# Performance work log

Measured on AMD Instinct MI355X. Metric: run time of the kernel, lower is better.

## Reference

```python
import jax, jax.numpy as jnp
import numpy as np

HEAD_NUM = 16
D_MODEL = 1024
D_K = D_MODEL // HEAD_NUM


def setup_inputs() -> dict:
    key = jax.random.key(0)
    ks = jax.random.split(key, 11)
    B, S = 4, 2048
    def xavier(k, shape):
        fan_in, fan_out = shape[1], shape[0]
        lim = np.sqrt(6.0 / (fan_in + fan_out))
        return jax.random.uniform(k, shape, jnp.float32, -lim, lim)
    return {
        "query": jax.random.normal(ks[0], (B, S, D_MODEL), jnp.float32),
        "key": jax.random.normal(ks[1], (B, S, D_MODEL), jnp.float32),
        "value": jax.random.normal(ks[2], (B, S, D_MODEL), jnp.float32),
        "w_q": xavier(ks[3], (D_MODEL, D_MODEL)),
        "b_q": jnp.zeros((D_MODEL,), jnp.float32),
        "w_k": xavier(ks[4], (D_MODEL, D_MODEL)),
        "b_k": jnp.zeros((D_MODEL,), jnp.float32),
        "w_v": xavier(ks[5], (D_MODEL, D_MODEL)),
        "b_v": jnp.zeros((D_MODEL,), jnp.float32),
        "w_o": xavier(ks[6], (D_MODEL, D_MODEL)),
        "b_o": jnp.zeros((D_MODEL,), jnp.float32),
    }


def reference(query, key, value, w_q, b_q, w_k, b_k, w_v, b_v, w_o, b_o):
    B = query.shape[0]
    # Linear projections (torch Linear: x @ W^T + b), split into heads: [B,H,S,Dk]
    def proj(x, w, b):
        y = x @ w.T + b
        return y.reshape(B, -1, HEAD_NUM, D_K).transpose(0, 2, 1, 3)
    q = proj(query, w_q, b_q)
    k = proj(key, w_k, b_k)
    v = proj(value, w_v, b_v)
    # scaled dot-product attention with full score matrix [B,H,Sq,Sk]
    scores = jnp.einsum('bhqd,bhkd->bhqk', q, k) / jnp.sqrt(jnp.float32(D_K))
    attn = jax.nn.softmax(scores, axis=-1)
    out = jnp.einsum('bhqk,bhkd->bhqd', attn, v)
    out = out.transpose(0, 2, 1, 3).reshape(B, -1, HEAD_NUM * D_K)
    return out @ w_o.T + b_o
```

## Files before the change

kernel.cpp:

```cpp
#include <hip/hip_runtime.h>
#include <hip/hip_bf16.h>
#include <stdint.h>

#define HN 16
#define DMODEL 1024
#define DKH 64
#define SEQ 2048

typedef __attribute__((ext_vector_type(8))) short short8v;
typedef __attribute__((ext_vector_type(4))) short short4v;
typedef __attribute__((ext_vector_type(4))) float f32x4;

__device__ __forceinline__ short bfc(float x) {
    __hip_bfloat16 h = __float2bfloat16(x);
    return *reinterpret_cast<short*>(&h);
}

__device__ __forceinline__ void gll16(const void* g, void* l) {
    __builtin_amdgcn_global_load_lds(
        (const __attribute__((address_space(1))) unsigned int*)g,
        (__attribute__((address_space(3))) unsigned int*)l, 16, 0, 0);
}

__global__ void cvtw_kernel(const float* __restrict__ w0, const float* __restrict__ w1,
                            const float* __restrict__ w2, const float* __restrict__ w3,
                            short* __restrict__ dst, float scale0) {
    const int z = blockIdx.z;
    const float* src = z == 0 ? w0 : z == 1 ? w1 : z == 2 ? w2 : w3;
    short* d = dst + ((size_t)z << 20);
    const float scale = (z == 0) ? scale0 : 1.f;
    const int i = blockIdx.x * blockDim.x + threadIdx.x;
    const float4 v0 = ((const float4*)src)[i * 2];
    const float4 v1 = ((const float4*)src)[i * 2 + 1];
    short8v o;
    o[0] = bfc(v0.x * scale); o[1] = bfc(v0.y * scale);
    o[2] = bfc(v0.z * scale); o[3] = bfc(v0.w * scale);
    o[4] = bfc(v1.x * scale); o[5] = bfc(v1.y * scale);
    o[6] = bfc(v1.z * scale); o[7] = bfc(v1.w * scale);
    ((short8v*)d)[i] = o;
}

__global__ __launch_bounds__(256) void gemm_proj(
    const float* __restrict__ xq, const float* __restrict__ xk, const float* __restrict__ xv,
    const short* __restrict__ wb,
    const float* __restrict__ bq, const float* __restrict__ bk, const float* __restrict__ bv,
    short* __restrict__ qb, short* __restrict__ kb, short* __restrict__ vtb, float c1)
{
    constexpr int K = DMODEL;
    const int z = blockIdx.z;
    const float* A    = z == 0 ? xq : z == 1 ? xk : xv;
    const short* W    = wb + ((size_t)z << 20);
    const float* bias = z == 0 ? bq : z == 1 ? bk : bv;
    const float bscale = (z == 0) ? c1 : 1.f;

    __shared__ __align__(16) short As[128][72];
    __shared__ __align__(16) short Bs[128][64];
    const int t = threadIdx.x, lane = t & 63;
    const int w = t >> 6, wr = w >> 1, wc = w & 1;
    const int m0 = blockIdx.y * 128, n0 = blockIdx.x * 128;
    const int r16 = lane & 15, g = lane >> 4;

    f32x4 acc[4][4];
    #pragma unroll
    for (int i = 0; i < 4; ++i)
        #pragma unroll
        for (int j = 0; j < 4; ++j) { acc[i][j][0]=0.f; acc[i][j][1]=0.f; acc[i][j][2]=0.f; acc[i][j][3]=0.f; }

    const int arow = t >> 1, acol = (t & 1) * 32;
    const float* Abase = A + (size_t)(m0 + arow) * K + acol;
    const int sr = t >> 3, sx = ((t & 7) ^ (sr & 7)) * 8;
    const short* Bbase = W + (size_t)(n0 + sr) * K + sx;
    short* lB = &Bs[0][0] + t * 8;

    for (int kt = 0; kt < K; kt += 64) {
        gll16(Bbase + kt,                  lB);
        gll16(Bbase + kt + (size_t)32 * K, lB + 2048);
        gll16(Bbase + kt + (size_t)64 * K, lB + 4096);
        gll16(Bbase + kt + (size_t)96 * K, lB + 6144);
        #pragma unroll
        for (int c = 0; c < 2; ++c) {
            float4 f0 = *(const float4*)(Abase + kt + c*16);
            float4 f1 = *(const float4*)(Abase + kt + c*16 + 4);
            float4 f2 = *(const float4*)(Abase + kt + c*16 + 8);
            float4 f3 = *(const float4*)(Abase + kt + c*16 + 12);
            short8v s0, s1;
            s0[0]=bfc(f0.x); s0[1]=bfc(f0.y); s0[2]=bfc(f0.z); s0[3]=bfc(f0.w);
            s0[4]=bfc(f1.x); s0[5]=bfc(f1.y); s0[6]=bfc(f1.z); s0[7]=bfc(f1.w);
            s1[0]=bfc(f2.x); s1[1]=bfc(f2.y); s1[2]=bfc(f2.z); s1[3]=bfc(f2.w);
            s1[4]=bfc(f3.x); s1[5]=bfc(f3.y); s1[6]=bfc(f3.z); s1[7]=bfc(f3.w);
            *(short8v*)&As[arow][acol + c*16]     = s0;
            *(short8v*)&As[arow][acol + c*16 + 8] = s1;
        }
        __syncthreads();
        #pragma unroll
        for (int kk = 0; kk < 2; ++kk) {
            short8v a[4], b[4];
            #pragma unroll
            for (int i = 0; i < 4; ++i)
                a[i] = *(const short8v*)&As[wr*64 + i*16 + r16][kk*32 + g*8];
            #pragma unroll
            for (int j = 0; j < 4; ++j)
                b[j] = *(const short8v*)&Bs[wc*64 + j*16 + r16][(((kk*4 + g) ^ (r16 & 7)) * 8)];
            #pragma unroll
            for (int i = 0; i < 4; ++i)
                #pragma unroll
                for (int j = 0; j < 4; ++j)
                    acc[i][j] = __builtin_amdgcn_mfma_f32_16x16x32_bf16(a[i], b[j], acc[i][j], 0, 0, 0);
        }
        __syncthreads();
    }

    #pragma unroll
    for (int i = 0; i < 4; ++i) {
        const int mbase = m0 + wr*64 + i*16 + g*4;
        #pragma unroll
        for (int j = 0; j < 4; ++j) {
            const int n = n0 + wc*64 + j*16 + r16;
            const float bvv = bias[n] * bscale;
            const int h = n >> 6, d = n & 63;
            if (z < 2) {
                short* ob = (z == 0) ? qb : kb;
                #pragma unroll
                for (int r = 0; r < 4; ++r) {
                    const int m = mbase + r;
                    const int bb = m >> 11, s = m & 2047;
                    ob[(((size_t)(bb*HN + h)*SEQ + s) << 6) + d] = bfc(acc[i][j][r] + bvv);
                }
            } else {
                const int bb = mbase >> 11, s = mbase & 2047;
                const int blk = s & ~31, b4 = (s >> 2) & 7;
                const int sp = blk | ((((b4 & 3) << 1) | (b4 >> 2)) << 2);
                short4v pk;
                #pragma unroll
                for (int r = 0; r < 4; ++r) pk[r] = bfc(acc[i][j][r] + bvv);
                *(short4v*)&vtb[((size_t)(bb*HN + h)*DKH + d)*SEQ + sp] = pk;
            }
        }
    }
}

__global__ __launch_bounds__(256, 2) void attn_kernel(
    const short* __restrict__ Qb, const short* __restrict__ Kb,
    const short* __restrict__ Vt, short* __restrict__ Ob)
{
    __shared__ __align__(16) short Ks[2][4096];
    __shared__ __align__(16) short Vs[2][4096];
    const int t = threadIdx.x, lane = t & 63, w = t >> 6;
    const int r16 = lane & 15, g = lane >> 4;
    const int bh = blockIdx.y;
    const size_t hq = (size_t)bh * SEQ * DKH;
    const size_t hv = (size_t)bh * DKH * SEQ;
    const int q0 = blockIdx.x * 256 + w * 64;

    short8v aq[4][2];
    #pragma unroll
    for (int qm = 0; qm < 4; ++qm)
        #pragma unroll
        for (int h2 = 0; h2 < 2; ++h2)
            aq[qm][h2] = *(const short8v*)(Qb + hq + (size_t)(q0 + qm*16 + r16)*DKH + h2*32 + g*8);

    short8v ones;
    #pragma unroll
    for (int j = 0; j < 8; ++j) ones[j] = (short)0x3F80;

    f32x4 o[4][4], ps[4];
    #pragma unroll
    for (int qm = 0; qm < 4; ++qm) {
        ps[qm][0]=0.f; ps[qm][1]=0.f; ps[qm][2]=0.f; ps[qm][3]=0.f;
        #pragma unroll
        for (int d = 0; d < 4; ++d) { o[qm][d][0]=0.f; o[qm][d][1]=0.f; o[qm][d][2]=0.f; o[qm][d][3]=0.f; }
    }
    const f32x4 zinit = {-4.f, -4.f, -4.f, -4.f};

    const int sr = t >> 3, sx = ((t & 7) ^ (sr & 7)) * 8;
    const short* Ksrc = Kb + hq + (size_t)sr * DKH + sx;
    const short* Vsrc = Vt + hv + (size_t)sr * SEQ + sx;
    const int l0 = t * 8, l1 = 2048 + t * 8;

    gll16(Ksrc,                    &Ks[0][l0]);
    gll16(Ksrc + (size_t)32*DKH,   &Ks[0][l1]);
    gll16(Vsrc,                    &Vs[0][l0]);
    gll16(Vsrc + (size_t)32*SEQ,   &Vs[0][l1]);
    __syncthreads();

    int cur = 0;
    for (int kv0 = 0; kv0 < SEQ; kv0 += 64) {
        if (kv0 + 64 < SEQ) {
            const int nxt = cur ^ 1;
            const int kn = kv0 + 64;
            gll16(Ksrc + (size_t)kn*DKH,        &Ks[nxt][l0]);
            gll16(Ksrc + (size_t)(kn+32)*DKH,   &Ks[nxt][l1]);
            gll16(Vsrc + kn,                    &Vs[nxt][l0]);
            gll16(Vsrc + (size_t)32*SEQ + kn,   &Vs[nxt][l1]);
        }
        const short* Kc = Ks[cur];
        const short* Vc = Vs[cur];

        short8v pa[4][2];
        #pragma unroll
        for (int s2 = 0; s2 < 4; ++s2) {
            const int krow = (s2*16 + r16) * 64;
            short8v ak0 = *(const short8v*)&Kc[krow + ((g       ^ (r16 & 7)) * 8)];
            short8v ak1 = *(const short8v*)&Kc[krow + (((4 + g) ^ (r16 & 7)) * 8)];
            #pragma unroll
            for (int qm = 0; qm < 4; ++qm) {
                f32x4 zz = __builtin_amdgcn_mfma_f32_16x16x32_bf16(ak0, aq[qm][0], zinit, 0, 0, 0);
                zz = __builtin_amdgcn_mfma_f32_16x16x32_bf16(ak1, aq[qm][1], zz, 0, 0, 0);
                pa[qm][s2 >> 1][(s2 & 1)*4 + 0] = bfc(exp2f(zz[0]));
                pa[qm][s2 >> 1][(s2 & 1)*4 + 1] = bfc(exp2f(zz[1]));
                pa[qm][s2 >> 1][(s2 & 1)*4 + 2] = bfc(exp2f(zz[2]));
                pa[qm][s2 >> 1][(s2 & 1)*4 + 3] = bfc(exp2f(zz[3]));
            }
        }
        #pragma unroll
        for (int kvh = 0; kvh < 2; ++kvh) {
            #pragma unroll
            for (int qm = 0; qm < 4; ++qm)
                ps[qm] = __builtin_amdgcn_mfma_f32_16x16x32_bf16(pa[qm][kvh], ones, ps[qm], 0, 0, 0);
            #pragma unroll
            for (int dblk = 0; dblk < 4; ++dblk) {
                short8v bvv = *(const short8v*)&Vc[(dblk*16 + r16)*64 + (((kvh*4 + g) ^ (r16 & 7)) * 8)];
                #pragma unroll
                for (int qm = 0; qm < 4; ++qm)
                    o[qm][dblk] = __builtin_amdgcn_mfma_f32_16x16x32_bf16(pa[qm][kvh], bvv, o[qm][dblk], 0, 0, 0);
            }
        }
        __syncthreads();
        cur ^= 1;
    }

    const int bb = bh >> 4, h = bh & 15;
    #pragma unroll
    for (int qm = 0; qm < 4; ++qm)
        #pragma unroll
        for (int r = 0; r < 4; ++r) {
            const float rp = 1.f / ps[qm][r];
            const int q = q0 + qm*16 + g*4 + r;
            #pragma unroll
            for (int dblk = 0; dblk < 4; ++dblk)
                Ob[(size_t)(bb*SEQ + q)*DMODEL + h*DKH + dblk*16 + r16] = bfc(o[qm][dblk][r] * rp);
        }
}

__global__ __launch_bounds__(256) void gemm_out(
    const short* __restrict__ Ain, const short* __restrict__ W,
    const float* __restrict__ bias, float* __restrict__ Out)
{
    constexpr int K = DMODEL;
    __shared__ __align__(16) short As[128][64];
    __shared__ __align__(16) short Bs[128][64];
    const int t = threadIdx.x, lane = t & 63;
    const int w = t >> 6, wr = w >> 1, wc = w & 1;
    const int m0 = blockIdx.y * 128, n0 = blockIdx.x * 128;
    const int r16 = lane & 15, g = lane >> 4;

    f32x4 acc[4][4];
    #pragma unroll
    for (int i = 0; i < 4; ++i)
        #pragma unroll
        for (int j = 0; j < 4; ++j) { acc[i][j][0]=0.f; acc[i][j][1]=0.f; acc[i][j][2]=0.f; acc[i][j][3]=0.f; }

    const int sr = t >> 3, sx = ((t & 7) ^ (sr & 7)) * 8;
    const short* Abase = Ain + (size_t)(m0 + sr) * K + sx;
    const short* Bbase = W   + (size_t)(n0 + sr) * K + sx;
    short* lA = &As[0][0] + t * 8;
    short* lB = &Bs[0][0] + t * 8;

    for (int kt = 0; kt < K; kt += 64) {
        #pragma unroll
        for (int q4 = 0; q4 < 4; ++q4) {
            gll16(Abase + kt + (size_t)(q4*32) * K, lA + q4*2048);
            gll16(Bbase + kt + (size_t)(q4*32) * K, lB + q4*2048);
        }
        __syncthreads();
        #pragma unroll
        for (int kk = 0; kk < 2; ++kk) {
            short8v a[4], b[4];
            #pragma unroll
            for (int i = 0; i < 4; ++i)
                a[i] = *(const short8v*)&As[wr*64 + i*16 + r16][(((kk*4 + g) ^ (r16 & 7)) * 8)];
            #pragma unroll
            for (int j = 0; j < 4; ++j)
                b[j] = *(const short8v*)&Bs[wc*64 + j*16 + r16][(((kk*4 + g) ^ (r16 & 7)) * 8)];
            #pragma unroll
            for (int i = 0; i < 4; ++i)
                #pragma unroll
                for (int j = 0; j < 4; ++j)
                    acc[i][j] = __builtin_amdgcn_mfma_f32_16x16x32_bf16(a[i], b[j], acc[i][j], 0, 0, 0);
        }
        __syncthreads();
    }

    #pragma unroll
    for (int i = 0; i < 4; ++i) {
        const int mbase = m0 + wr*64 + i*16 + g*4;
        #pragma unroll
        for (int j = 0; j < 4; ++j) {
            const int n = n0 + wc*64 + j*16 + r16;
            const float bvv = bias[n];
            #pragma unroll
            for (int r = 0; r < 4; ++r)
                Out[(size_t)(mbase + r)*DMODEL + n] = acc[i][j][r] + bvv;
        }
    }
}

extern "C" void kernel_launch(void* const* d_in, const int* in_sizes, int n_in,
                              void* d_out, int out_size, void* d_ws, size_t ws_size,
                              hipStream_t stream) {
    const float* query = (const float*)d_in[0];
    const float* key   = (const float*)d_in[1];
    const float* value = (const float*)d_in[2];
    const float* w_q = (const float*)d_in[3];
    const float* b_q = (const float*)d_in[4];
    const float* w_k = (const float*)d_in[5];
    const float* b_k = (const float*)d_in[6];
    const float* w_v = (const float*)d_in[7];
    const float* b_v = (const float*)d_in[8];
    const float* w_o = (const float*)d_in[9];
    const float* b_o = (const float*)d_in[10];

    const float C1 = 0.18033688011112043f;

    short* ws  = (short*)d_ws;
    short* wb  = ws;
    short* qb  = ws + (4u  << 20);
    short* kb  = ws + (12u << 20);
    short* vtb = ws + (20u << 20);
    short* xb  = ws + (28u << 20);

    cvtw_kernel<<<dim3(512, 1, 4), 256, 0, stream>>>(w_q, w_k, w_v, w_o, wb, C1);

    gemm_proj<<<dim3(8, 64, 3), 256, 0, stream>>>(query, key, value, wb,
                                                  b_q, b_k, b_v, qb, kb, vtb, C1);

    attn_kernel<<<dim3(8, 64), 256, 0, stream>>>(qb, kb, vtb, xb);

    gemm_out<<<dim3(8, 64), 256, 0, stream>>>(xb, wb + (3u << 20), b_o, (float*)d_out);
}
```

Before: 399.1 us.

## Pre-convert activations to bf16 and double-buffer LDS loads in both GEMMs

New measurement: 357.9 us. 10.3% less time.

```diff
diff --git a/kernel.cpp b/kernel.cpp
--- a/kernel.cpp
+++ b/kernel.cpp
@@ -40,21 +40,36 @@
     ((short8v*)d)[i] = o;
 }
 
+__global__ void cvtx_kernel(const float* __restrict__ x0, const float* __restrict__ x1,
+                            const float* __restrict__ x2, short* __restrict__ dst,
+                            unsigned zstride) {
+    const int z = blockIdx.z;
+    const float* src = z == 0 ? x0 : z == 1 ? x1 : x2;
+    short* d = dst + (size_t)z * zstride;
+    const int i = blockIdx.x * blockDim.x + threadIdx.x;
+    const float4 v0 = ((const float4*)src)[i * 2];
+    const float4 v1 = ((const float4*)src)[i * 2 + 1];
+    short8v o;
+    o[0] = bfc(v0.x); o[1] = bfc(v0.y); o[2] = bfc(v0.z); o[3] = bfc(v0.w);
+    o[4] = bfc(v1.x); o[5] = bfc(v1.y); o[6] = bfc(v1.z); o[7] = bfc(v1.w);
+    ((short8v*)d)[i] = o;
+}
+
 __global__ __launch_bounds__(256) void gemm_proj(
-    const float* __restrict__ xq, const float* __restrict__ xk, const float* __restrict__ xv,
+    const short* __restrict__ Ax, unsigned zstride, int z0,
     const short* __restrict__ wb,
     const float* __restrict__ bq, const float* __restrict__ bk, const float* __restrict__ bv,
     short* __restrict__ qb, short* __restrict__ kb, short* __restrict__ vtb, float c1)
 {
     constexpr int K = DMODEL;
-    const int z = blockIdx.z;
-    const float* A    = z == 0 ? xq : z == 1 ? xk : xv;
+    const int z = z0 + blockIdx.z;
+    const short* A    = Ax + (size_t)blockIdx.z * zstride;
     const short* W    = wb + ((size_t)z << 20);
     const float* bias = z == 0 ? bq : z == 1 ? bk : bv;
     const float bscale = (z == 0) ? c1 : 1.f;
 
-    __shared__ __align__(16) short As[128][72];
-    __shared__ __align__(16) short Bs[128][64];
+    __shared__ __align__(16) short As[2][8192];
+    __shared__ __align__(16) short Bs[2][8192];
     const int t = threadIdx.x, lane = t & 63;
     const int w = t >> 6, wr = w >> 1, wc = w & 1;
     const int m0 = blockIdx.y * 128, n0 = blockIdx.x * 128;
@@ -66,41 +81,38 @@
         #pragma unroll
         for (int j = 0; j < 4; ++j) { acc[i][j][0]=0.f; acc[i][j][1]=0.f; acc[i][j][2]=0.f; acc[i][j][3]=0.f; }
 
-    const int arow = t >> 1, acol = (t & 1) * 32;
-    const float* Abase = A + (size_t)(m0 + arow) * K + acol;
     const int sr = t >> 3, sx = ((t & 7) ^ (sr & 7)) * 8;
-    const short* Bbase = W + (size_t)(n0 + sr) * K + sx;
-    short* lB = &Bs[0][0] + t * 8;
-
+    const short* Asrc = A + (size_t)(m0 + sr) * K + sx;
+    const short* Bsrc = W + (size_t)(n0 + sr) * K + sx;
+
+    #pragma unroll
+    for (int q4 = 0; q4 < 4; ++q4) {
+        gll16(Asrc + (size_t)(q4*32) * K, &As[0][0] + t*8 + q4*2048);
+        gll16(Bsrc + (size_t)(q4*32) * K, &Bs[0][0] + t*8 + q4*2048);
+    }
+    __syncthreads();
+
+    int cur = 0;
     for (int kt = 0; kt < K; kt += 64) {
-        gll16(Bbase + kt,                  lB);
-        gll16(Bbase + kt + (size_t)32 * K, lB + 2048);
-        gll16(Bbase + kt + (size_t)64 * K, lB + 4096);
-        gll16(Bbase + kt + (size_t)96 * K, lB + 6144);
-        #pragma unroll
-        for (int c = 0; c < 2; ++c) {
-            float4 f0 = *(const float4*)(Abase + kt + c*16);
-            float4 f1 = *(const float4*)(Abase + kt + c*16 + 4);
-            float4 f2 = *(const float4*)(Abase + kt + c*16 + 8);
-            float4 f3 = *(const float4*)(Abase + kt + c*16 + 12);
-            short8v s0, s1;
-            s0[0]=bfc(f0.x); s0[1]=bfc(f0.y); s0[2]=bfc(f0.z); s0[3]=bfc(f0.w);
-            s0[4]=bfc(f1.x); s0[5]=bfc(f1.y); s0[6]=bfc(f1.z); s0[7]=bfc(f1.w);
-            s1[0]=bfc(f2.x); s1[1]=bfc(f2.y); s1[2]=bfc(f2.z); s1[3]=bfc(f2.w);
-            s1[4]=bfc(f3.x); s1[5]=bfc(f3.y); s1[6]=bfc(f3.z); s1[7]=bfc(f3.w);
-            *(short8v*)&As[arow][acol + c*16]     = s0;
-            *(short8v*)&As[arow][acol + c*16 + 8] = s1;
-        }
-        __syncthreads();
+        if (kt + 64 < K) {
+            const int nxt = cur ^ 1;
+            #pragma unroll
+            for (int q4 = 0; q4 < 4; ++q4) {
+                gll16(Asrc + kt + 64 + (size_t)(q4*32) * K, &As[nxt][0] + t*8 + q4*2048);
+                gll16(Bsrc + kt + 64 + (size_t)(q4*32) * K, &Bs[nxt][0] + t*8 + q4*2048);
+            }
+        }
+        const short* Ac = As[cur];
+        const short* Bc = Bs[cur];
         #pragma unroll
         for (int kk = 0; kk < 2; ++kk) {
             short8v a[4], b[4];
             #pragma unroll
             for (int i = 0; i < 4; ++i)
-                a[i] = *(const short8v*)&As[wr*64 + i*16 + r16][kk*32 + g*8];
+                a[i] = *(const short8v*)&Ac[(wr*64 + i*16 + r16)*64 + (((kk*4 + g) ^ (r16 & 7)) * 8)];
             #pragma unroll
             for (int j = 0; j < 4; ++j)
-                b[j] = *(const short8v*)&Bs[wc*64 + j*16 + r16][(((kk*4 + g) ^ (r16 & 7)) * 8)];
+                b[j] = *(const short8v*)&Bc[(wc*64 + j*16 + r16)*64 + (((kk*4 + g) ^ (r16 & 7)) * 8)];
             #pragma unroll
             for (int i = 0; i < 4; ++i)
                 #pragma unroll
@@ -108,6 +120,7 @@
                     acc[i][j] = __builtin_amdgcn_mfma_f32_16x16x32_bf16(a[i], b[j], acc[i][j], 0, 0, 0);
         }
         __syncthreads();
+        cur ^= 1;
     }
 
     #pragma unroll
@@ -247,8 +260,8 @@
     const float* __restrict__ bias, float* __restrict__ Out)
 {
     constexpr int K = DMODEL;
-    __shared__ __align__(16) short As[128][64];
-    __shared__ __align__(16) short Bs[128][64];
+    __shared__ __align__(16) short As[2][8192];
+    __shared__ __align__(16) short Bs[2][8192];
     const int t = threadIdx.x, lane = t & 63;
     const int w = t >> 6, wr = w >> 1, wc = w & 1;
     const int m0 = blockIdx.y * 128, n0 = blockIdx.x * 128;
@@ -261,27 +274,37 @@
         for (int j = 0; j < 4; ++j) { acc[i][j][0]=0.f; acc[i][j][1]=0.f; acc[i][j][2]=0.f; acc[i][j][3]=0.f; }
 
     const int sr = t >> 3, sx = ((t & 7) ^ (sr & 7)) * 8;
-    const short* Abase = Ain + (size_t)(m0 + sr) * K + sx;
-    const short* Bbase = W   + (size_t)(n0 + sr) * K + sx;
-    short* lA = &As[0][0] + t * 8;
-    short* lB = &Bs[0][0] + t * 8;
-
+    const short* Asrc = Ain + (size_t)(m0 + sr) * K + sx;
+    const short* Bsrc = W   + (size_t)(n0 + sr) * K + sx;
+
+    #pragma unroll
+    for (int q4 = 0; q4 < 4; ++q4) {
+        gll16(Asrc + (size_t)(q4*32) * K, &As[0][0] + t*8 + q4*2048);
+        gll16(Bsrc + (size_t)(q4*32) * K, &Bs[0][0] + t*8 + q4*2048);
+    }
+    __syncthreads();
+
+    int cur = 0;
     for (int kt = 0; kt < K; kt += 64) {
-        #pragma unroll
-        for (int q4 = 0; q4 < 4; ++q4) {
-            gll16(Abase + kt + (size_t)(q4*32) * K, lA + q4*2048);
-            gll16(Bbase + kt + (size_t)(q4*32) * K, lB + q4*2048);
-        }
-        __syncthreads();
+        if (kt + 64 < K) {
+            const int nxt = cur ^ 1;
+            #pragma unroll
+            for (int q4 = 0; q4 < 4; ++q4) {
+                gll16(Asrc + kt + 64 + (size_t)(q4*32) * K, &As[nxt][0] + t*8 + q4*2048);
+                gll16(Bsrc + kt + 64 + (size_t)(q4*32) * K, &Bs[nxt][0] + t*8 + q4*2048);
+            }
+        }
+        const short* Ac = As[cur];
+        const short* Bc = Bs[cur];
         #pragma unroll
         for (int kk = 0; kk < 2; ++kk) {
             short8v a[4], b[4];
             #pragma unroll
             for (int i = 0; i < 4; ++i)
-                a[i] = *(const short8v*)&As[wr*64 + i*16 + r16][(((kk*4 + g) ^ (r16 & 7)) * 8)];
+                a[i] = *(const short8v*)&Ac[(wr*64 + i*16 + r16)*64 + (((kk*4 + g) ^ (r16 & 7)) * 8)];
             #pragma unroll
             for (int j = 0; j < 4; ++j)
-                b[j] = *(const short8v*)&Bs[wc*64 + j*16 + r16][(((kk*4 + g) ^ (r16 & 7)) * 8)];
+                b[j] = *(const short8v*)&Bc[(wc*64 + j*16 + r16)*64 + (((kk*4 + g) ^ (r16 & 7)) * 8)];
             #pragma unroll
             for (int i = 0; i < 4; ++i)
                 #pragma unroll
@@ -289,6 +312,7 @@
                     acc[i][j] = __builtin_amdgcn_mfma_f32_16x16x32_bf16(a[i], b[j], acc[i][j], 0, 0, 0);
         }
         __syncthreads();
+        cur ^= 1;
     }
 
     #pragma unroll
@@ -322,19 +346,41 @@
 
     const float C1 = 0.18033688011112043f;
 
-    short* ws  = (short*)d_ws;
-    short* wb  = ws;
-    short* qb  = ws + (4u  << 20);
-    short* kb  = ws + (12u << 20);
-    short* vtb = ws + (20u << 20);
-    short* xb  = ws + (28u << 20);
+    short* ws = (short*)d_ws;
+    short* wb = ws;
+    short* xo = ws + (4u << 20);
+
+    const bool fused = ws_size >= (size_t)104 * 1024 * 1024;
+    short *xq, *qb, *kb, *vtb;
+    if (fused) {
+        xq  = ws + (4u  << 20);
+        qb  = ws + (28u << 20);
+        kb  = ws + (36u << 20);
+        vtb = ws + (44u << 20);
+    } else {
+        xq  = ws + (4u  << 20);
+        qb  = ws + (12u << 20);
+        kb  = ws + (20u << 20);
+        vtb = ws + (28u << 20);
+    }
 
     cvtw_kernel<<<dim3(512, 1, 4), 256, 0, stream>>>(w_q, w_k, w_v, w_o, wb, C1);
 
-    gemm_proj<<<dim3(8, 64, 3), 256, 0, stream>>>(query, key, value, wb,
-                                                  b_q, b_k, b_v, qb, kb, vtb, C1);
-
-    attn_kernel<<<dim3(8, 64), 256, 0, stream>>>(qb, kb, vtb, xb);
-
-    gemm_out<<<dim3(8, 64), 256, 0, stream>>>(xb, wb + (3u << 20), b_o, (float*)d_out);
-}
+    if (fused) {
+        cvtx_kernel<<<dim3(4096, 1, 3), 256, 0, stream>>>(query, key, value, xq, 1u << 23);
+        gemm_proj<<<dim3(8, 64, 3), 256, 0, stream>>>(xq, 1u << 23, 0, wb,
+                                                      b_q, b_k, b_v, qb, kb, vtb, C1);
+    } else {
+        const float* xs0 = query; const float* xs1 = key; const float* xs2 = value;
+        const float* xs[3] = {xs0, xs1, xs2};
+        for (int z = 0; z < 3; ++z) {
+            cvtx_kernel<<<dim3(4096, 1, 1), 256, 0, stream>>>(xs[z], xs[z], xs[z], xq, 0);
+            gemm_proj<<<dim3(8, 64, 1), 256, 0, stream>>>(xq, 0, z, wb,
+                                                          b_q, b_k, b_v, qb, kb, vtb, C1);
+        }
+    }
+
+    attn_kernel<<<dim3(8, 64), 256, 0, stream>>>(qb, kb, vtb, xo);
+
+    gemm_out<<<dim3(8, 64), 256, 0, stream>>>(xo, wb + (3u << 20), b_o, (float*)d_out);
+}
```
